# Kernel optimization log

Measured on AMD Instinct MI355X. Metric: run time of the kernel, lower is better.

## Reference

```python
import jax, jax.numpy as jnp
import numpy as np

H = 2048   # hidden_size
I = 4096   # intermediate_size (expert_dim_per_shard, world_size=1)
E = 8      # num_local_experts


def setup_inputs() -> dict:
    key = jax.random.key(0)
    ks = jax.random.split(key, 7)
    s = 0.02
    return {
        "hidden_states": jax.random.normal(ks[0], (1, 2048, H), dtype=jnp.float32),
        "router_w": jax.random.normal(ks[1], (H, E), dtype=jnp.float32) * s,
        "gate_up_proj": jax.random.normal(ks[2], (E, H, 2 * I), dtype=jnp.float32) * s,
        "down_proj": jax.random.normal(ks[3], (E, I, H), dtype=jnp.float32) * s,
        "shared_gate_w": jax.random.normal(ks[4], (H, I), dtype=jnp.float32) * s,
        "shared_up_w": jax.random.normal(ks[5], (H, I), dtype=jnp.float32) * s,
        "shared_down_w": jax.random.normal(ks[6], (I, H), dtype=jnp.float32) * s,
        "top_k": 1,
    }


def reference(hidden_states, router_w, gate_up_proj, down_proj,
              shared_gate_w, shared_up_w, shared_down_w, top_k):
    b, s, h = hidden_states.shape
    hs = hidden_states.reshape(-1, h)                      # [T, H]
    T = hs.shape[0]

    # router + topk scatter (non-topk -> -inf so sigmoid -> 0)
    logits = hs @ router_w                                 # [T, E]
    top_v, top_i = jax.lax.top_k(logits, top_k)            # [T, k]
    neg_inf = jnp.full_like(logits, -jnp.inf)
    rows = jnp.arange(T)[:, None]
    router_scores = neg_inf.at[rows, top_i].set(top_v).T   # [E, T]
    router_scores = jax.nn.sigmoid(router_scores.astype(jnp.float32)).astype(hs.dtype)

    # dense dispatch: every token to every expert, scaled by (mostly zero) scores
    routed_in = hs[None, :, :] * router_scores[:, :, None]  # [E, T, H]

    # per-expert grouped GEMM (SwiGLU)
    gate_up = jnp.einsum('eth,ehf->etf', routed_in, gate_up_proj)  # [E, T, 2I]
    gate, up = jnp.split(gate_up, 2, axis=-1)
    routed_out = jnp.einsum('eti,eih->eth', up * jax.nn.silu(gate), down_proj)  # [E, T, H]

    # shared expert (SwiGLU MLP)
    shared = (jax.nn.silu(hs @ shared_gate_w) * (hs @ shared_up_w)) @ shared_down_w  # [T, H]

    # scatter_add over arange indices == sum over experts
    out = shared + routed_out.sum(axis=0)                  # [T, H]
    return out, router_scores
```

## Files before the change

### kernel.cpp

```cpp
#include <hip/hip_runtime.h>
#include <hip/hip_bf16.h>

#define H_DIM 2048
#define E_NUM 8
#define I_DIM 4096
#define TWO_I 8192
#define T_TOK 2048

#define BM 256
#define BN 64
#define BK 64

typedef __bf16 bf16x8 __attribute__((ext_vector_type(8)));
typedef float f32x4 __attribute__((ext_vector_type(4)));

static __device__ __forceinline__ unsigned short f2bs(float x) {
    __hip_bfloat16 h = __float2bfloat16(x);
    return __builtin_bit_cast(unsigned short, h);
}

#define GLL(gsrc, ldst) __builtin_amdgcn_global_load_lds( \
    (const __attribute__((address_space(1))) void*)(gsrc), \
    (__attribute__((address_space(3))) void*)(ldst), 16, 0, 0)

#define BSWZ(n) (((((n) & 7) ^ (((n) >> 2) & 7))) << 4)

#define A_SRC_CHUNK(lane) ((((lane) & 7) ^ (((lane) >> 3) & 7)) * 8)

static __device__ __forceinline__ void stage_b(
    const float* __restrict__ src, size_t ldb, unsigned short* __restrict__ Bs,
    int wave, int lane) {
    int k0 = wave * 16 + ((lane >> 4) << 2);
    int nb = (lane & 15) << 2;
    const float* p = src + (size_t)k0 * ldb + nb;
    float4 r0 = *reinterpret_cast<const float4*>(p);
    float4 r1 = *reinterpret_cast<const float4*>(p + ldb);
    float4 r2 = *reinterpret_cast<const float4*>(p + 2 * (size_t)ldb);
    float4 r3 = *reinterpret_cast<const float4*>(p + 3 * (size_t)ldb);
    ushort4 o;
    int n, off;
    n = nb + 0;
    o.x = f2bs(r0.x); o.y = f2bs(r1.x); o.z = f2bs(r2.x); o.w = f2bs(r3.x);
    off = (n * 128 + k0 * 2) ^ BSWZ(n);
    *reinterpret_cast<ushort4*>((char*)Bs + off) = o;
    n = nb + 1;
    o.x = f2bs(r0.y); o.y = f2bs(r1.y); o.z = f2bs(r2.y); o.w = f2bs(r3.y);
    off = (n * 128 + k0 * 2) ^ BSWZ(n);
    *reinterpret_cast<ushort4*>((char*)Bs + off) = o;
    n = nb + 2;
    o.x = f2bs(r0.z); o.y = f2bs(r1.z); o.z = f2bs(r2.z); o.w = f2bs(r3.z);
    off = (n * 128 + k0 * 2) ^ BSWZ(n);
    *reinterpret_cast<ushort4*>((char*)Bs + off) = o;
    n = nb + 3;
    o.x = f2bs(r0.w); o.y = f2bs(r1.w); o.z = f2bs(r2.w); o.w = f2bs(r3.w);
    off = (n * 128 + k0 * 2) ^ BSWZ(n);
    *reinterpret_cast<ushort4*>((char*)Bs + off) = o;
}

static __device__ __forceinline__ bf16x8 bload(
    const unsigned short* __restrict__ Bs, int n, int s, int h) {
    int off = (n * 128 + s * 64 + h * 16) ^ BSWZ(n);
    return *reinterpret_cast<const bf16x8*>((const char*)Bs + off);
}

static __device__ __forceinline__ bf16x8 aload(
    const unsigned short* __restrict__ As, int row, int s, int h) {
    int off = row * 128 + ((s * 64 + h * 16) ^ ((row & 7) << 4));
    return *reinterpret_cast<const bf16x8*>((const char*)As + off);
}

__global__ __launch_bounds__(256) void router_convert_kernel(
    const float* __restrict__ hs, const float* __restrict__ rw,
    float* __restrict__ out_scores, int* __restrict__ eidx,
    unsigned short* __restrict__ xb, unsigned short* __restrict__ xs) {
    int tok = blockIdx.x * 4 + (threadIdx.x >> 6);
    int lane = threadIdx.x & 63;
    const float* row = hs + (size_t)tok * H_DIM;
    float4 v[8];
    float acc[E_NUM];
#pragma unroll
    for (int e = 0; e < E_NUM; e++) acc[e] = 0.f;
#pragma unroll
    for (int i = 0; i < 8; i++) {
        int hb = i * 256 + lane * 4;
        v[i] = *reinterpret_cast<const float4*>(row + hb);
        const float* w0 = rw + (size_t)hb * E_NUM;
#pragma unroll
        for (int e = 0; e < E_NUM; e++) {
            acc[e] += v[i].x * w0[e] + v[i].y * w0[E_NUM + e] +
                      v[i].z * w0[2 * E_NUM + e] + v[i].w * w0[3 * E_NUM + e];
        }
    }
#pragma unroll
    for (int e = 0; e < E_NUM; e++) {
#pragma unroll
        for (int o = 32; o > 0; o >>= 1) acc[e] += __shfl_xor(acc[e], o, 64);
    }
    int best = 0; float bv = acc[0];
#pragma unroll
    for (int e = 1; e < E_NUM; e++) { if (acc[e] > bv) { bv = acc[e]; best = e; } }
    float sc = 1.f / (1.f + expf(-bv));
    if (lane < E_NUM) out_scores[(size_t)lane * T_TOK + tok] = (lane == best) ? sc : 0.f;
    if (lane == 0) eidx[tok] = best;
    unsigned short* xbr = xb + (size_t)tok * H_DIM;
    unsigned short* xsr = xs + (size_t)tok * H_DIM;
#pragma unroll
    for (int i = 0; i < 8; i++) {
        int hb = i * 256 + lane * 4;
        ushort4 b, s4;
        b.x = f2bs(v[i].x); b.y = f2bs(v[i].y); b.z = f2bs(v[i].z); b.w = f2bs(v[i].w);
        s4.x = f2bs(v[i].x * sc); s4.y = f2bs(v[i].y * sc);
        s4.z = f2bs(v[i].z * sc); s4.w = f2bs(v[i].w * sc);
        *reinterpret_cast<ushort4*>(xbr + hb) = b;
        *reinterpret_cast<ushort4*>(xsr + hb) = s4;
    }
}

__global__ void group_kernel(const int* __restrict__ eidx, int* __restrict__ perm,
                             int* __restrict__ off) {
    __shared__ int cnt[E_NUM];
    __shared__ int base[E_NUM];
    int t = threadIdx.x;
    if (t < E_NUM) cnt[t] = 0;
    __syncthreads();
    for (int i = t; i < T_TOK; i += 256) atomicAdd(&cnt[eidx[i]], 1);
    __syncthreads();
    if (t == 0) {
        int s = 0;
        for (int e = 0; e < E_NUM; e++) { base[e] = s; off[e] = s; s += cnt[e]; }
        off[E_NUM] = s;
    }
    __syncthreads();
    for (int i = t; i < T_TOK; i += 256) {
        int e = eidx[i];
        int p = atomicAdd(&base[e], 1);
        perm[p] = i;
    }
}

__global__ __launch_bounds__(256, 2) void gemm1_kernel(
    const unsigned short* __restrict__ xb, const unsigned short* __restrict__ xs,
    const float* __restrict__ gup, const float* __restrict__ sg,
    const float* __restrict__ su, const int* __restrict__ perm,
    const int* __restrict__ off, unsigned short* __restrict__ hmid) {
    int nt = blockIdx.x;
    int g = blockIdx.y >> 3;
    int mt = blockIdx.y & 7;
    int rowbase, ng;
    if (g < E_NUM) { rowbase = off[g]; ng = off[g + 1] - rowbase; }
    else { rowbase = 0; ng = T_TOK; }
    int mstart = mt * BM;
    if (mstart >= ng) return;

    __shared__ unsigned short As[BM][BK];
    __shared__ unsigned short Bg[BN * BK];
    __shared__ unsigned short Bu[BN * BK];

    int tid = threadIdx.x;
    int wave = tid >> 6, lane = tid & 63;
    int h = lane >> 4, ln = lane & 15;

    const unsigned short* Abase = (g == E_NUM) ? xb : xs;
    unsigned int aoff[8];
#pragma unroll
    for (int j = 0; j < 8; j++) {
        int r = wave * 64 + j * 8 + (lane >> 3);
        int sr = mstart + r; sr = (sr < ng) ? sr : (ng - 1);
        int tokr = (g < E_NUM) ? perm[rowbase + sr] : sr;
        aoff[j] = (unsigned int)tokr * H_DIM + A_SRC_CHUNK(lane);
    }
    int n0 = nt * BN;
    const float* gbase;
    const float* ubase;
    size_t ldb;
    if (g < E_NUM) {
        gbase = gup + (size_t)g * H_DIM * TWO_I + n0;
        ubase = gbase + I_DIM;
        ldb = TWO_I;
    } else {
        gbase = sg + n0;
        ubase = su + n0;
        ldb = I_DIM;
    }

    f32x4 zero = {0.f, 0.f, 0.f, 0.f};
    f32x4 accg[4][4], accu[4][4];
#pragma unroll
    for (int i = 0; i < 4; i++)
#pragma unroll
        for (int j = 0; j < 4; j++) { accg[i][j] = zero; accu[i][j] = zero; }

    for (int k0 = 0; k0 < H_DIM; k0 += BK) {
#pragma unroll
        for (int j = 0; j < 8; j++) GLL(Abase + aoff[j] + k0, &As[wave * 64 + j * 8][0]);
        stage_b(gbase + (size_t)k0 * ldb, ldb, Bg, wave, lane);
        stage_b(ubase + (size_t)k0 * ldb, ldb, Bu, wave, lane);
        __syncthreads();
#pragma unroll
        for (int s = 0; s < 2; s++) {
            bf16x8 a[4];
#pragma unroll
            for (int i = 0; i < 4; i++)
                a[i] = aload(&As[0][0], wave * 64 + i * 16 + ln, s, h);
#pragma unroll
            for (int j = 0; j < 4; j++) {
                bf16x8 bg = bload(Bg, j * 16 + ln, s, h);
#pragma unroll
                for (int i = 0; i < 4; i++)
                    accg[i][j] = __builtin_amdgcn_mfma_f32_16x16x32_bf16(a[i], bg, accg[i][j], 0, 0, 0);
            }
#pragma unroll
            for (int j = 0; j < 4; j++) {
                bf16x8 bu = bload(Bu, j * 16 + ln, s, h);
#pragma unroll
                for (int i = 0; i < 4; i++)
                    accu[i][j] = __builtin_amdgcn_mfma_f32_16x16x32_bf16(a[i], bu, accu[i][j], 0, 0, 0);
            }
        }
        __syncthreads();
    }
    int hbase = (g < E_NUM) ? rowbase : T_TOK;
#pragma unroll
    for (int i = 0; i < 4; i++) {
#pragma unroll
        for (int j = 0; j < 4; j++) {
#pragma unroll
            for (int r = 0; r < 4; r++) {
                int row = wave * 64 + i * 16 + h * 4 + r;
                int sr = mstart + row;
                if (sr < ng) {
                    float gv = accg[i][j][r], uv = accu[i][j][r];
                    float hv = gv / (1.f + expf(-gv)) * uv;
                    int col = n0 + j * 16 + ln;
                    hmid[(size_t)(hbase + sr) * I_DIM + col] = f2bs(hv);
                }
            }
        }
    }
}

template <int ADD>
__global__ __launch_bounds__(256, 2) void gemm2_kernel(
    const unsigned short* __restrict__ hmid, const float* __restrict__ dwn,
    const float* __restrict__ sd, const int* __restrict__ perm,
    const int* __restrict__ off, float* __restrict__ out) {
    int nt = blockIdx.x;
    int g, mt, rowbase, ng, hbase;
    if (ADD) {
        g = blockIdx.y >> 3; mt = blockIdx.y & 7;
        rowbase = off[g]; ng = off[g + 1] - rowbase; hbase = rowbase;
    } else {
        g = E_NUM; mt = blockIdx.y; rowbase = 0; ng = T_TOK; hbase = T_TOK;
    }
    int mstart = mt * BM;
    if (mstart >= ng) return;

    __shared__ unsigned short As[BM][BK];
    __shared__ unsigned short Bs[BN * BK];

    int tid = threadIdx.x;
    int wave = tid >> 6, lane = tid & 63;
    int h = lane >> 4, ln = lane & 15;

    unsigned int aoff[8];
#pragma unroll
    for (int j = 0; j < 8; j++) {
        int r = wave * 64 + j * 8 + (lane >> 3);
        int sr = mstart + r; sr = (sr < ng) ? sr : (ng - 1);
        aoff[j] = (unsigned int)(hbase + sr) * I_DIM + A_SRC_CHUNK(lane);
    }
    int n0 = nt * BN;
    const float* bbase = ADD ? (dwn + (size_t)g * I_DIM * H_DIM + n0) : (sd + n0);

    f32x4 zero = {0.f, 0.f, 0.f, 0.f};
    f32x4 acc[4][4];
#pragma unroll
    for (int i = 0; i < 4; i++)
#pragma unroll
        for (int j = 0; j < 4; j++) acc[i][j] = zero;

    for (int k0 = 0; k0 < I_DIM; k0 += BK) {
#pragma unroll
        for (int j = 0; j < 8; j++) GLL(hmid + aoff[j] + k0, &As[wave * 64 + j * 8][0]);
        stage_b(bbase + (size_t)k0 * H_DIM, H_DIM, Bs, wave, lane);
        __syncthreads();
#pragma unroll
        for (int s = 0; s < 2; s++) {
            bf16x8 a[4];
#pragma unroll
            for (int i = 0; i < 4; i++)
                a[i] = aload(&As[0][0], wave * 64 + i * 16 + ln, s, h);
#pragma unroll
            for (int j = 0; j < 4; j++) {
                bf16x8 b = bload(Bs, j * 16 + ln, s, h);
#pragma unroll
                for (int i = 0; i < 4; i++)
                    acc[i][j] = __builtin_amdgcn_mfma_f32_16x16x32_bf16(a[i], b, acc[i][j], 0, 0, 0);
            }
        }
        __syncthreads();
    }
#pragma unroll
    for (int i = 0; i < 4; i++) {
#pragma unroll
        for (int j = 0; j < 4; j++) {
#pragma unroll
            for (int r = 0; r < 4; r++) {
                int row = wave * 64 + i * 16 + h * 4 + r;
                int sr = mstart + row;
                if (sr < ng) {
                    int tok = ADD ? perm[rowbase + sr] : sr;
                    int col = n0 + j * 16 + ln;
                    float v = acc[i][j][r];
                    float* o = out + (size_t)tok * H_DIM + col;
                    if (ADD) *o += v; else *o = v;
                }
            }
        }
    }
}

extern "C" void kernel_launch(void* const* d_in, const int* in_sizes, int n_in,
                              void* d_out, int out_size, void* d_ws, size_t ws_size,
                              hipStream_t stream) {
    (void)in_sizes; (void)n_in; (void)out_size;
    const float* hs  = (const float*)d_in[0];
    const float* rw  = (const float*)d_in[1];
    const float* gup = (const float*)d_in[2];
    const float* dwn = (const float*)d_in[3];
    const float* sg  = (const float*)d_in[4];
    const float* su  = (const float*)d_in[5];
    const float* sd  = (const float*)d_in[6];
    float* out = (float*)d_out;
    float* out_scores = out + (size_t)T_TOK * H_DIM;

    char* w = (char*)d_ws;
    size_t o = 0;
    auto alloc = [&](size_t bytes) {
        void* p = w + o;
        o += (bytes + 255) & ~(size_t)255;
        return p;
    };
    unsigned short* xb   = (unsigned short*)alloc((size_t)T_TOK * H_DIM * 2);
    unsigned short* xs   = (unsigned short*)alloc((size_t)T_TOK * H_DIM * 2);
    unsigned short* hmid = (unsigned short*)alloc((size_t)2 * T_TOK * I_DIM * 2);
    int* eidx    = (int*)alloc(T_TOK * 4);
    int* perm    = (int*)alloc(T_TOK * 4);
    int* off     = (int*)alloc(64 * 4);
    if (ws_size < o) return;

    router_convert_kernel<<<T_TOK / 4, 256, 0, stream>>>(hs, rw, out_scores, eidx, xb, xs);
    group_kernel<<<1, 256, 0, stream>>>(eidx, perm, off);

    gemm1_kernel<<<dim3(I_DIM / BN, 9 * 8), 256, 0, stream>>>(
        xb, xs, gup, sg, su, perm, off, hmid);
    gemm2_kernel<0><<<dim3(H_DIM / BN, 8), 256, 0, stream>>>(hmid, dwn, sd, perm, off, out);
    gemm2_kernel<1><<<dim3(H_DIM / BN, E_NUM * 8), 256, 0, stream>>>(hmid, dwn, sd, perm, off, out);
}
```

Baseline: 583.5 us.

## Double-buffer GEMM shared tiles with register prefetch and 512-thread blocks

```diff
diff --git a/kernel.cpp b/kernel.cpp
--- a/kernel.cpp
+++ b/kernel.cpp
@@ -7,10 +7,6 @@
 #define TWO_I 8192
 #define T_TOK 2048
 
-#define BM 256
-#define BN 64
-#define BK 64
-
 typedef __bf16 bf16x8 __attribute__((ext_vector_type(8)));
 typedef float f32x4 __attribute__((ext_vector_type(4)));
 
@@ -24,38 +20,7 @@
     (__attribute__((address_space(3))) void*)(ldst), 16, 0, 0)
 
 #define BSWZ(n) (((((n) & 7) ^ (((n) >> 2) & 7))) << 4)
-
 #define A_SRC_CHUNK(lane) ((((lane) & 7) ^ (((lane) >> 3) & 7)) * 8)
-
-static __device__ __forceinline__ void stage_b(
-    const float* __restrict__ src, size_t ldb, unsigned short* __restrict__ Bs,
-    int wave, int lane) {
-    int k0 = wave * 16 + ((lane >> 4) << 2);
-    int nb = (lane & 15) << 2;
-    const float* p = src + (size_t)k0 * ldb + nb;
-    float4 r0 = *reinterpret_cast<const float4*>(p);
-    float4 r1 = *reinterpret_cast<const float4*>(p + ldb);
-    float4 r2 = *reinterpret_cast<const float4*>(p + 2 * (size_t)ldb);
-    float4 r3 = *reinterpret_cast<const float4*>(p + 3 * (size_t)ldb);
-    ushort4 o;
-    int n, off;
-    n = nb + 0;
-    o.x = f2bs(r0.x); o.y = f2bs(r1.x); o.z = f2bs(r2.x); o.w = f2bs(r3.x);
-    off = (n * 128 + k0 * 2) ^ BSWZ(n);
-    *reinterpret_cast<ushort4*>((char*)Bs + off) = o;
-    n = nb + 1;
-    o.x = f2bs(r0.y); o.y = f2bs(r1.y); o.z = f2bs(r2.y); o.w = f2bs(r3.y);
-    off = (n * 128 + k0 * 2) ^ BSWZ(n);
-    *reinterpret_cast<ushort4*>((char*)Bs + off) = o;
-    n = nb + 2;
-    o.x = f2bs(r0.z); o.y = f2bs(r1.z); o.z = f2bs(r2.z); o.w = f2bs(r3.z);
-    off = (n * 128 + k0 * 2) ^ BSWZ(n);
-    *reinterpret_cast<ushort4*>((char*)Bs + off) = o;
-    n = nb + 3;
-    o.x = f2bs(r0.w); o.y = f2bs(r1.w); o.z = f2bs(r2.w); o.w = f2bs(r3.w);
-    off = (n * 128 + k0 * 2) ^ BSWZ(n);
-    *reinterpret_cast<ushort4*>((char*)Bs + off) = o;
-}
 
 static __device__ __forceinline__ bf16x8 bload(
     const unsigned short* __restrict__ Bs, int n, int s, int h) {
@@ -68,6 +33,8 @@
     int off = row * 128 + ((s * 64 + h * 16) ^ ((row & 7) << 4));
     return *reinterpret_cast<const bf16x8*>((const char*)As + off);
 }
+
+#define MFMA16(a, b, c) __builtin_amdgcn_mfma_f32_16x16x32_bf16(a, b, c, 0, 0, 0)
 
 __global__ __launch_bounds__(256) void router_convert_kernel(
     const float* __restrict__ hs, const float* __restrict__ rw,
@@ -138,7 +105,7 @@
     }
 }
 
-__global__ __launch_bounds__(256, 2) void gemm1_kernel(
+__global__ __launch_bounds__(512, 2) void gemm1_kernel(
     const unsigned short* __restrict__ xb, const unsigned short* __restrict__ xs,
     const float* __restrict__ gup, const float* __restrict__ sg,
     const float* __restrict__ su, const int* __restrict__ perm,
@@ -149,27 +116,28 @@
     int rowbase, ng;
     if (g < E_NUM) { rowbase = off[g]; ng = off[g + 1] - rowbase; }
     else { rowbase = 0; ng = T_TOK; }
-    int mstart = mt * BM;
+    int mstart = mt * 256;
     if (mstart >= ng) return;
 
-    __shared__ unsigned short As[BM][BK];
-    __shared__ unsigned short Bg[BN * BK];
-    __shared__ unsigned short Bu[BN * BK];
+    __shared__ unsigned short As[2][256 * 64];
+    __shared__ unsigned short Bgs[2][64 * 64];
+    __shared__ unsigned short Bus[2][64 * 64];
 
     int tid = threadIdx.x;
     int wave = tid >> 6, lane = tid & 63;
+    int wr = wave >> 1, wc = wave & 1;
     int h = lane >> 4, ln = lane & 15;
 
     const unsigned short* Abase = (g == E_NUM) ? xb : xs;
-    unsigned int aoff[8];
-#pragma unroll
-    for (int j = 0; j < 8; j++) {
-        int r = wave * 64 + j * 8 + (lane >> 3);
+    unsigned int aoff[4];
+#pragma unroll
+    for (int j = 0; j < 4; j++) {
+        int r = wave * 32 + j * 8 + (lane >> 3);
         int sr = mstart + r; sr = (sr < ng) ? sr : (ng - 1);
         int tokr = (g < E_NUM) ? perm[rowbase + sr] : sr;
         aoff[j] = (unsigned int)tokr * H_DIM + A_SRC_CHUNK(lane);
     }
-    int n0 = nt * BN;
+    int n0 = nt * 64;
     const float* gbase;
     const float* ubase;
     size_t ldb;
@@ -182,56 +150,90 @@
         ubase = su + n0;
         ldb = I_DIM;
     }
+    const float* bsrc = (wave < 4) ? gbase : ubase;
+    int bk0 = (wave & 3) * 16 + ((lane >> 4) << 2);
+    int bnb = (lane & 15) << 2;
+    const float* bp = bsrc + (size_t)bk0 * ldb + bnb;
 
     f32x4 zero = {0.f, 0.f, 0.f, 0.f};
-    f32x4 accg[4][4], accu[4][4];
+    f32x4 accg[4][2], accu[4][2];
 #pragma unroll
     for (int i = 0; i < 4; i++)
 #pragma unroll
-        for (int j = 0; j < 4; j++) { accg[i][j] = zero; accu[i][j] = zero; }
-
-    for (int k0 = 0; k0 < H_DIM; k0 += BK) {
-#pragma unroll
-        for (int j = 0; j < 8; j++) GLL(Abase + aoff[j] + k0, &As[wave * 64 + j * 8][0]);
-        stage_b(gbase + (size_t)k0 * ldb, ldb, Bg, wave, lane);
-        stage_b(ubase + (size_t)k0 * ldb, ldb, Bu, wave, lane);
-        __syncthreads();
+        for (int j = 0; j < 2; j++) { accg[i][j] = zero; accu[i][j] = zero; }
+
+    f32x4 q0, q1, q2, q3;
+    const int NT = H_DIM / 64;
+
+#define G1_BLOAD(t) { const float* p_ = bp + (size_t)(t) * 64 * ldb; \
+        q0 = *reinterpret_cast<const f32x4*>(p_); \
+        q1 = *reinterpret_cast<const f32x4*>(p_ + ldb); \
+        q2 = *reinterpret_cast<const f32x4*>(p_ + 2 * ldb); \
+        q3 = *reinterpret_cast<const f32x4*>(p_ + 3 * ldb); }
+#define G1_BWRITE(buf) { char* bdst_ = (char*)((wave < 4) ? &Bgs[buf][0] : &Bus[buf][0]); \
+        _Pragma("unroll") \
+        for (int i_ = 0; i_ < 4; i_++) { int n_ = bnb + i_; ushort4 o_; \
+            o_.x = f2bs(q0[i_]); o_.y = f2bs(q1[i_]); o_.z = f2bs(q2[i_]); o_.w = f2bs(q3[i_]); \
+            int ob_ = (n_ * 128 + bk0 * 2) ^ BSWZ(n_); \
+            *reinterpret_cast<ushort4*>(bdst_ + ob_) = o_; } }
+#define G1_AGLL(t, buf) { _Pragma("unroll") \
+        for (int j_ = 0; j_ < 4; j_++) \
+            GLL(Abase + aoff[j_] + (t) * 64, &As[buf][(wave * 32 + j_ * 8) * 64]); }
+
+    G1_BLOAD(0);
+    G1_AGLL(0, 0);
+    asm volatile("s_waitcnt vmcnt(0)" ::: "memory");
+    G1_BWRITE(0);
+    G1_BLOAD(1);
+    asm volatile("s_waitcnt lgkmcnt(0)" ::: "memory");
+    __builtin_amdgcn_s_barrier();
+
+    int cur = 0;
+    for (int t = 0; t < NT; ++t) {
+        int tn1 = (t + 1 < NT) ? t + 1 : NT - 1;
+        int tn2 = (t + 2 < NT) ? t + 2 : NT - 1;
+        G1_BWRITE(cur ^ 1);
+        G1_AGLL(tn1, cur ^ 1);
+        G1_BLOAD(tn2);
 #pragma unroll
         for (int s = 0; s < 2; s++) {
             bf16x8 a[4];
 #pragma unroll
             for (int i = 0; i < 4; i++)
-                a[i] = aload(&As[0][0], wave * 64 + i * 16 + ln, s, h);
-#pragma unroll
-            for (int j = 0; j < 4; j++) {
-                bf16x8 bg = bload(Bg, j * 16 + ln, s, h);
-#pragma unroll
-                for (int i = 0; i < 4; i++)
-                    accg[i][j] = __builtin_amdgcn_mfma_f32_16x16x32_bf16(a[i], bg, accg[i][j], 0, 0, 0);
+                a[i] = aload(&As[cur][0], wr * 64 + i * 16 + ln, s, h);
+            bf16x8 bg0 = bload(&Bgs[cur][0], wc * 32 + ln, s, h);
+            bf16x8 bg1 = bload(&Bgs[cur][0], wc * 32 + 16 + ln, s, h);
+            bf16x8 bu0 = bload(&Bus[cur][0], wc * 32 + ln, s, h);
+            bf16x8 bu1 = bload(&Bus[cur][0], wc * 32 + 16 + ln, s, h);
+            __builtin_amdgcn_s_setprio(1);
+#pragma unroll
+            for (int i = 0; i < 4; i++) {
+                accg[i][0] = MFMA16(a[i], bg0, accg[i][0]);
+                accg[i][1] = MFMA16(a[i], bg1, accg[i][1]);
+                accu[i][0] = MFMA16(a[i], bu0, accu[i][0]);
+                accu[i][1] = MFMA16(a[i], bu1, accu[i][1]);
             }
-#pragma unroll
-            for (int j = 0; j < 4; j++) {
-                bf16x8 bu = bload(Bu, j * 16 + ln, s, h);
-#pragma unroll
-                for (int i = 0; i < 4; i++)
-                    accu[i][j] = __builtin_amdgcn_mfma_f32_16x16x32_bf16(a[i], bu, accu[i][j], 0, 0, 0);
-            }
+            __builtin_amdgcn_s_setprio(0);
         }
-        __syncthreads();
-    }
+        asm volatile("s_waitcnt vmcnt(4)" ::: "memory");
+        asm volatile("s_waitcnt lgkmcnt(0)" ::: "memory");
+        __builtin_amdgcn_s_barrier();
+        cur ^= 1;
+    }
+
     int hbase = (g < E_NUM) ? rowbase : T_TOK;
 #pragma unroll
     for (int i = 0; i < 4; i++) {
 #pragma unroll
-        for (int j = 0; j < 4; j++) {
+        for (int jj = 0; jj < 2; jj++) {
 #pragma unroll
             for (int r = 0; r < 4; r++) {
-                int row = wave * 64 + i * 16 + h * 4 + r;
+                int row = wr * 64 + i * 16 + h * 4 + r;
                 int sr = mstart + row;
                 if (sr < ng) {
-                    float gv = accg[i][j][r], uv = accu[i][j][r];
+                    float gv = accg[i][jj][r], uv = accu[i][jj][r];
                     float hv = gv / (1.f + expf(-gv)) * uv;
-                    int col = n0 + j * 16 + ln;
+                    int col = n0 + wc * 32 + jj * 16 + ln;
                     hmid[(size_t)(hbase + sr) * I_DIM + col] = f2bs(hv);
                 }
             }
@@ -240,7 +242,7 @@
 }
 
 template <int ADD>
-__global__ __launch_bounds__(256, 2) void gemm2_kernel(
+__global__ __launch_bounds__(512, 2) void gemm2_kernel(
     const unsigned short* __restrict__ hmid, const float* __restrict__ dwn,
     const float* __restrict__ sd, const int* __restrict__ perm,
     const int* __restrict__ off, float* __restrict__ out) {
@@ -252,25 +254,29 @@
     } else {
         g = E_NUM; mt = blockIdx.y; rowbase = 0; ng = T_TOK; hbase = T_TOK;
     }
-    int mstart = mt * BM;
+    int mstart = mt * 256;
     if (mstart >= ng) return;
 
-    __shared__ unsigned short As[BM][BK];
-    __shared__ unsigned short Bs[BN * BK];
+    __shared__ unsigned short As[2][256 * 64];
+    __shared__ unsigned short Bs[2][128 * 64];
 
     int tid = threadIdx.x;
     int wave = tid >> 6, lane = tid & 63;
+    int wr = wave >> 1, wc = wave & 1;
     int h = lane >> 4, ln = lane & 15;
 
-    unsigned int aoff[8];
-#pragma unroll
-    for (int j = 0; j < 8; j++) {
-        int r = wave * 64 + j * 8 + (lane >> 3);
+    unsigned int aoff[4];
+#pragma unroll
+    for (int j = 0; j < 4; j++) {
+        int r = wave * 32 + j * 8 + (lane >> 3);
         int sr = mstart + r; sr = (sr < ng) ? sr : (ng - 1);
         aoff[j] = (unsigned int)(hbase + sr) * I_DIM + A_SRC_CHUNK(lane);
     }
-    int n0 = nt * BN;
+    int n0 = nt * 128;
     const float* bbase = ADD ? (dwn + (size_t)g * I_DIM * H_DIM + n0) : (sd + n0);
+    int bk0 = ((tid >> 5) & 15) * 4;
+    int bnb = (tid & 31) * 4;
+    const float* bp = bbase + (size_t)bk0 * H_DIM + bnb;
 
     f32x4 zero = {0.f, 0.f, 0.f, 0.f};
     f32x4 acc[4][4];
@@ -279,38 +285,74 @@
 #pragma unroll
         for (int j = 0; j < 4; j++) acc[i][j] = zero;
 
-    for (int k0 = 0; k0 < I_DIM; k0 += BK) {
-#pragma unroll
-        for (int j = 0; j < 8; j++) GLL(hmid + aoff[j] + k0, &As[wave * 64 + j * 8][0]);
-        stage_b(bbase + (size_t)k0 * H_DIM, H_DIM, Bs, wave, lane);
-        __syncthreads();
+    f32x4 q0, q1, q2, q3;
+    const int NT = I_DIM / 64;
+
+#define G2_BLOAD(t) { const float* p_ = bp + (size_t)(t) * 64 * H_DIM; \
+        q0 = *reinterpret_cast<const f32x4*>(p_); \
+        q1 = *reinterpret_cast<const f32x4*>(p_ + H_DIM); \
+        q2 = *reinterpret_cast<const f32x4*>(p_ + 2 * H_DIM); \
+        q3 = *reinterpret_cast<const f32x4*>(p_ + 3 * H_DIM); }
+#define G2_BWRITE(buf) { char* bdst_ = (char*)&Bs[buf][0]; \
+        _Pragma("unroll") \
+        for (int i_ = 0; i_ < 4; i_++) { int n_ = bnb + i_; ushort4 o_; \
+            o_.x = f2bs(q0[i_]); o_.y = f2bs(q1[i_]); o_.z = f2bs(q2[i_]); o_.w = f2bs(q3[i_]); \
+            int ob_ = (n_ * 128 + bk0 * 2) ^ BSWZ(n_); \
+            *reinterpret_cast<ushort4*>(bdst_ + ob_) = o_; } }
+#define G2_AGLL(t, buf) { _Pragma("unroll") \
+        for (int j_ = 0; j_ < 4; j_++) \
+            GLL(hmid + aoff[j_] + (t) * 64, &As[buf][(wave * 32 + j_ * 8) * 64]); }
+
+    G2_BLOAD(0);
+    G2_AGLL(0, 0);
+    asm volatile("s_waitcnt vmcnt(0)" ::: "memory");
+    G2_BWRITE(0);
+    G2_BLOAD(1);
+    asm volatile("s_waitcnt lgkmcnt(0)" ::: "memory");
+    __builtin_amdgcn_s_barrier();
+
+    int cur = 0;
+    for (int t = 0; t < NT; ++t) {
+        int tn1 = (t + 1 < NT) ? t + 1 : NT - 1;
+        int tn2 = (t + 2 < NT) ? t + 2 : NT - 1;
+        G2_BWRITE(cur ^ 1);
+        G2_AGLL(tn1, cur ^ 1);
+        G2_BLOAD(tn2);
 #pragma unroll
         for (int s = 0; s < 2; s++) {
             bf16x8 a[4];
 #pragma unroll
             for (int i = 0; i < 4; i++)
-                a[i] = aload(&As[0][0], wave * 64 + i * 16 + ln, s, h);
-#pragma unroll
-            for (int j = 0; j < 4; j++) {
-                bf16x8 b = bload(Bs, j * 16 + ln, s, h);
+                a[i] = aload(&As[cur][0], wr * 64 + i * 16 + ln, s, h);
+            bf16x8 b[4];
+#pragma unroll
+            for (int j = 0; j < 4; j++)
+                b[j] = bload(&Bs[cur][0], wc * 64 + j * 16 + ln, s, h);
+            __builtin_amdgcn_s_setprio(1);
+#pragma unroll
+            for (int j = 0; j < 4; j++)
 #pragma unroll
                 for (int i = 0; i < 4; i++)
-                    acc[i][j] = __builtin_amdgcn_mfma_f32_16x16x32_bf16(a[i], b, acc[i][j], 0, 0, 0);
-            }
+                    acc[i][j] = MFMA16(a[i], b[j], acc[i][j]);
+            __builtin_amdgcn_s_setprio(0);
         }
-        __syncthreads();
-    }
+        asm volatile("s_waitcnt vmcnt(4)" ::: "memory");
+        asm volatile("s_waitcnt lgkmcnt(0)" ::: "memory");
+        __builtin_amdgcn_s_barrier();
+        cur ^= 1;
+    }
+
 #pragma unroll
     for (int i = 0; i < 4; i++) {
 #pragma unroll
         for (int j = 0; j < 4; j++) {
 #pragma unroll
             for (int r = 0; r < 4; r++) {
-                int row = wave * 64 + i * 16 + h * 4 + r;
+                int row = wr * 64 + i * 16 + h * 4 + r;
                 int sr = mstart + row;
                 if (sr < ng) {
                     int tok = ADD ? perm[rowbase + sr] : sr;
-                    int col = n0 + j * 16 + ln;
+                    int col = n0 + wc * 64 + j * 16 + ln;
                     float v = acc[i][j][r];
                     float* o = out + (size_t)tok * H_DIM + col;
                     if (ADD) *o += v; else *o = v;
@@ -352,8 +394,8 @@
     router_convert_kernel<<<T_TOK / 4, 256, 0, stream>>>(hs, rw, out_scores, eidx, xb, xs);
     group_kernel<<<1, 256, 0, stream>>>(eidx, perm, off);
 
-    gemm1_kernel<<<dim3(I_DIM / BN, 9 * 8), 256, 0, stream>>>(
+    gemm1_kernel<<<dim3(I_DIM / 64, 9 * 8), 512, 0, stream>>>(
         xb, xs, gup, sg, su, perm, off, hmid);
-    gemm2_kernel<0><<<dim3(H_DIM / BN, 8), 256, 0, stream>>>(hmid, dwn, sd, perm, off, out);
-    gemm2_kernel<1><<<dim3(H_DIM / BN, E_NUM * 8), 256, 0, stream>>>(hmid, dwn, sd, perm, off, out);
-}
+    gemm2_kernel<0><<<dim3(H_DIM / 128, 8), 512, 0, stream>>>(hmid, dwn, sd, perm, off, out);
+    gemm2_kernel<1><<<dim3(H_DIM / 128, E_NUM * 8), 512, 0, stream>>>(hmid, dwn, sd, perm, off, out);
+}
```

Result: slower. 636.9 us (+9.2%).

## Replace LDS-staged GEMMs with direct-to-register loads and register prefetch

Applied to the files above, without the earlier changes.

```diff
diff --git a/kernel.cpp b/kernel.cpp
--- a/kernel.cpp
+++ b/kernel.cpp
@@ -7,10 +7,6 @@
 #define TWO_I 8192
 #define T_TOK 2048
 
-#define BM 256
-#define BN 64
-#define BK 64
-
 typedef __bf16 bf16x8 __attribute__((ext_vector_type(8)));
 typedef float f32x4 __attribute__((ext_vector_type(4)));
 
@@ -19,55 +15,17 @@
     return __builtin_bit_cast(unsigned short, h);
 }
 
-#define GLL(gsrc, ldst) __builtin_amdgcn_global_load_lds( \
-    (const __attribute__((address_space(1))) void*)(gsrc), \
-    (__attribute__((address_space(3))) void*)(ldst), 16, 0, 0)
-
-#define BSWZ(n) (((((n) & 7) ^ (((n) >> 2) & 7))) << 4)
-
-#define A_SRC_CHUNK(lane) ((((lane) & 7) ^ (((lane) >> 3) & 7)) * 8)
-
-static __device__ __forceinline__ void stage_b(
-    const float* __restrict__ src, size_t ldb, unsigned short* __restrict__ Bs,
-    int wave, int lane) {
-    int k0 = wave * 16 + ((lane >> 4) << 2);
-    int nb = (lane & 15) << 2;
-    const float* p = src + (size_t)k0 * ldb + nb;
-    float4 r0 = *reinterpret_cast<const float4*>(p);
-    float4 r1 = *reinterpret_cast<const float4*>(p + ldb);
-    float4 r2 = *reinterpret_cast<const float4*>(p + 2 * (size_t)ldb);
-    float4 r3 = *reinterpret_cast<const float4*>(p + 3 * (size_t)ldb);
-    ushort4 o;
-    int n, off;
-    n = nb + 0;
-    o.x = f2bs(r0.x); o.y = f2bs(r1.x); o.z = f2bs(r2.x); o.w = f2bs(r3.x);
-    off = (n * 128 + k0 * 2) ^ BSWZ(n);
-    *reinterpret_cast<ushort4*>((char*)Bs + off) = o;
-    n = nb + 1;
-    o.x = f2bs(r0.y); o.y = f2bs(r1.y); o.z = f2bs(r2.y); o.w = f2bs(r3.y);
-    off = (n * 128 + k0 * 2) ^ BSWZ(n);
-    *reinterpret_cast<ushort4*>((char*)Bs + off) = o;
-    n = nb + 2;
-    o.x = f2bs(r0.z); o.y = f2bs(r1.z); o.z = f2bs(r2.z); o.w = f2bs(r3.z);
-    off = (n * 128 + k0 * 2) ^ BSWZ(n);
-    *reinterpret_cast<ushort4*>((char*)Bs + off) = o;
-    n = nb + 3;
-    o.x = f2bs(r0.w); o.y = f2bs(r1.w); o.z = f2bs(r2.w); o.w = f2bs(r3.w);
-    off = (n * 128 + k0 * 2) ^ BSWZ(n);
-    *reinterpret_cast<ushort4*>((char*)Bs + off) = o;
-}
-
-static __device__ __forceinline__ bf16x8 bload(
-    const unsigned short* __restrict__ Bs, int n, int s, int h) {
-    int off = (n * 128 + s * 64 + h * 16) ^ BSWZ(n);
-    return *reinterpret_cast<const bf16x8*>((const char*)Bs + off);
-}
-
-static __device__ __forceinline__ bf16x8 aload(
-    const unsigned short* __restrict__ As, int row, int s, int h) {
-    int off = row * 128 + ((s * 64 + h * 16) ^ ((row & 7) << 4));
-    return *reinterpret_cast<const bf16x8*>((const char*)As + off);
-}
+static __device__ __forceinline__ bf16x8 cvt8(const float* q) {
+    bf16x8 r;
+#pragma unroll
+    for (int j = 0; j < 8; j++) r[j] = (__bf16)q[j];
+    return r;
+}
+
+#define MFMA16(a, b, c) __builtin_amdgcn_mfma_f32_16x16x32_bf16(a, b, c, 0, 0, 0)
+
+#define LDQ(dst, p, kk) { _Pragma("unroll") \
+    for (int j_ = 0; j_ < 8; j_++) dst[j_] = (p)[(kk) + (size_t)j_ * ldb]; }
 
 __global__ __launch_bounds__(256) void router_convert_kernel(
     const float* __restrict__ hs, const float* __restrict__ rw,
@@ -138,101 +96,90 @@
     }
 }
 
-__global__ __launch_bounds__(256, 2) void gemm1_kernel(
+__global__ __launch_bounds__(256, 3) void gemm1_kernel(
     const unsigned short* __restrict__ xb, const unsigned short* __restrict__ xs,
     const float* __restrict__ gup, const float* __restrict__ sg,
     const float* __restrict__ su, const int* __restrict__ perm,
     const int* __restrict__ off, unsigned short* __restrict__ hmid) {
     int nt = blockIdx.x;
-    int g = blockIdx.y >> 3;
-    int mt = blockIdx.y & 7;
+    int g = blockIdx.y >> 4;
+    int mt = blockIdx.y & 15;
     int rowbase, ng;
     if (g < E_NUM) { rowbase = off[g]; ng = off[g + 1] - rowbase; }
     else { rowbase = 0; ng = T_TOK; }
-    int mstart = mt * BM;
+    int mstart = mt * 128;
     if (mstart >= ng) return;
-
-    __shared__ unsigned short As[BM][BK];
-    __shared__ unsigned short Bg[BN * BK];
-    __shared__ unsigned short Bu[BN * BK];
 
     int tid = threadIdx.x;
     int wave = tid >> 6, lane = tid & 63;
-    int h = lane >> 4, ln = lane & 15;
+    int wr = wave >> 1, wc = wave & 1;
+    int ln = lane & 15, h = lane >> 4;
 
     const unsigned short* Abase = (g == E_NUM) ? xb : xs;
-    unsigned int aoff[8];
-#pragma unroll
-    for (int j = 0; j < 8; j++) {
-        int r = wave * 64 + j * 8 + (lane >> 3);
-        int sr = mstart + r; sr = (sr < ng) ? sr : (ng - 1);
-        int tokr = (g < E_NUM) ? perm[rowbase + sr] : sr;
-        aoff[j] = (unsigned int)tokr * H_DIM + A_SRC_CHUNK(lane);
-    }
-    int n0 = nt * BN;
-    const float* gbase;
-    const float* ubase;
-    size_t ldb;
-    if (g < E_NUM) {
-        gbase = gup + (size_t)g * H_DIM * TWO_I + n0;
-        ubase = gbase + I_DIM;
-        ldb = TWO_I;
-    } else {
-        gbase = sg + n0;
-        ubase = su + n0;
-        ldb = I_DIM;
-    }
+    int mbase = mstart + wr * 64;
+    unsigned aoff0, aoff1, aoff2, aoff3;
+#define MKAOFF1(i, dst) { int r_ = mbase + i * 16 + ln; r_ = (r_ < ng) ? r_ : (ng - 1); \
+        int tok_ = (g < E_NUM) ? perm[rowbase + r_] : r_; dst = (unsigned)tok_ * H_DIM + h * 8; }
+    MKAOFF1(0, aoff0) MKAOFF1(1, aoff1) MKAOFF1(2, aoff2) MKAOFF1(3, aoff3)
+
+    const float* gbase; const float* ubase; size_t ldb;
+    if (g < E_NUM) { gbase = gup + (size_t)g * H_DIM * TWO_I; ubase = gbase + I_DIM; ldb = TWO_I; }
+    else { gbase = sg; ubase = su; ldb = I_DIM; }
+    int colg = nt * 64 + wc * 32 + ln;
+    const float* pg0 = gbase + (size_t)(h * 8) * ldb + colg;
+    const float* pg1 = pg0 + 16;
+    const float* pu0 = ubase + (size_t)(h * 8) * ldb + colg;
+    const float* pu1 = pu0 + 16;
 
     f32x4 zero = {0.f, 0.f, 0.f, 0.f};
-    f32x4 accg[4][4], accu[4][4];
+    f32x4 accg[4][2], accu[4][2];
 #pragma unroll
     for (int i = 0; i < 4; i++)
 #pragma unroll
-        for (int j = 0; j < 4; j++) { accg[i][j] = zero; accu[i][j] = zero; }
-
-    for (int k0 = 0; k0 < H_DIM; k0 += BK) {
-#pragma unroll
-        for (int j = 0; j < 8; j++) GLL(Abase + aoff[j] + k0, &As[wave * 64 + j * 8][0]);
-        stage_b(gbase + (size_t)k0 * ldb, ldb, Bg, wave, lane);
-        stage_b(ubase + (size_t)k0 * ldb, ldb, Bu, wave, lane);
-        __syncthreads();
-#pragma unroll
-        for (int s = 0; s < 2; s++) {
-            bf16x8 a[4];
-#pragma unroll
-            for (int i = 0; i < 4; i++)
-                a[i] = aload(&As[0][0], wave * 64 + i * 16 + ln, s, h);
-#pragma unroll
-            for (int j = 0; j < 4; j++) {
-                bf16x8 bg = bload(Bg, j * 16 + ln, s, h);
-#pragma unroll
-                for (int i = 0; i < 4; i++)
-                    accg[i][j] = __builtin_amdgcn_mfma_f32_16x16x32_bf16(a[i], bg, accg[i][j], 0, 0, 0);
-            }
-#pragma unroll
-            for (int j = 0; j < 4; j++) {
-                bf16x8 bu = bload(Bu, j * 16 + ln, s, h);
-#pragma unroll
-                for (int i = 0; i < 4; i++)
-                    accu[i][j] = __builtin_amdgcn_mfma_f32_16x16x32_bf16(a[i], bu, accu[i][j], 0, 0, 0);
-            }
-        }
-        __syncthreads();
-    }
+        for (int j = 0; j < 2; j++) { accg[i][j] = zero; accu[i][j] = zero; }
+
+    float qg0[8], qg1[8], qu0[8], qu1[8];
+    bf16x8 aq0, aq1, aq2, aq3;
+    const int NT = H_DIM / 32;
+
+    LDQ(qg0, pg0, 0); LDQ(qg1, pg1, 0); LDQ(qu0, pu0, 0); LDQ(qu1, pu1, 0);
+    aq0 = *(const bf16x8*)(Abase + aoff0);
+    aq1 = *(const bf16x8*)(Abase + aoff1);
+    aq2 = *(const bf16x8*)(Abase + aoff2);
+    aq3 = *(const bf16x8*)(Abase + aoff3);
+
+    for (int t = 0; t < NT; ++t) {
+        bf16x8 bg0 = cvt8(qg0), bg1 = cvt8(qg1), bu0 = cvt8(qu0), bu1 = cvt8(qu1);
+        bf16x8 a0 = aq0, a1 = aq1, a2 = aq2, a3 = aq3;
+        int tn = (t + 1 < NT) ? (t + 1) : t;
+        size_t kk = (size_t)tn * 32 * ldb;
+        unsigned ka = (unsigned)tn * 32;
+        LDQ(qg0, pg0, kk); LDQ(qg1, pg1, kk); LDQ(qu0, pu0, kk); LDQ(qu1, pu1, kk);
+        aq0 = *(const bf16x8*)(Abase + aoff0 + ka);
+        aq1 = *(const bf16x8*)(Abase + aoff1 + ka);
+        aq2 = *(const bf16x8*)(Abase + aoff2 + ka);
+        aq3 = *(const bf16x8*)(Abase + aoff3 + ka);
+#define G1_ROW(i, ai) \
+        accg[i][0] = MFMA16(ai, bg0, accg[i][0]); \
+        accg[i][1] = MFMA16(ai, bg1, accg[i][1]); \
+        accu[i][0] = MFMA16(ai, bu0, accu[i][0]); \
+        accu[i][1] = MFMA16(ai, bu1, accu[i][1]);
+        G1_ROW(0, a0) G1_ROW(1, a1) G1_ROW(2, a2) G1_ROW(3, a3)
+    }
+
     int hbase = (g < E_NUM) ? rowbase : T_TOK;
 #pragma unroll
     for (int i = 0; i < 4; i++) {
 #pragma unroll
-        for (int j = 0; j < 4; j++) {
+        for (int jn = 0; jn < 2; jn++) {
 #pragma unroll
             for (int r = 0; r < 4; r++) {
-                int row = wave * 64 + i * 16 + h * 4 + r;
-                int sr = mstart + row;
-                if (sr < ng) {
-                    float gv = accg[i][j][r], uv = accu[i][j][r];
+                int row = mbase + i * 16 + h * 4 + r;
+                if (row < ng) {
+                    float gv = accg[i][jn][r], uv = accu[i][jn][r];
                     float hv = gv / (1.f + expf(-gv)) * uv;
-                    int col = n0 + j * 16 + ln;
-                    hmid[(size_t)(hbase + sr) * I_DIM + col] = f2bs(hv);
+                    int col = nt * 64 + wc * 32 + jn * 16 + ln;
+                    hmid[(size_t)(hbase + row) * I_DIM + col] = f2bs(hv);
                 }
             }
         }
@@ -240,37 +187,39 @@
 }
 
 template <int ADD>
-__global__ __launch_bounds__(256, 2) void gemm2_kernel(
+__global__ __launch_bounds__(256, 3) void gemm2_kernel(
     const unsigned short* __restrict__ hmid, const float* __restrict__ dwn,
     const float* __restrict__ sd, const int* __restrict__ perm,
     const int* __restrict__ off, float* __restrict__ out) {
     int nt = blockIdx.x;
     int g, mt, rowbase, ng, hbase;
     if (ADD) {
-        g = blockIdx.y >> 3; mt = blockIdx.y & 7;
+        g = blockIdx.y >> 4; mt = blockIdx.y & 15;
         rowbase = off[g]; ng = off[g + 1] - rowbase; hbase = rowbase;
     } else {
         g = E_NUM; mt = blockIdx.y; rowbase = 0; ng = T_TOK; hbase = T_TOK;
     }
-    int mstart = mt * BM;
+    int mstart = mt * 128;
     if (mstart >= ng) return;
-
-    __shared__ unsigned short As[BM][BK];
-    __shared__ unsigned short Bs[BN * BK];
 
     int tid = threadIdx.x;
     int wave = tid >> 6, lane = tid & 63;
-    int h = lane >> 4, ln = lane & 15;
-
-    unsigned int aoff[8];
-#pragma unroll
-    for (int j = 0; j < 8; j++) {
-        int r = wave * 64 + j * 8 + (lane >> 3);
-        int sr = mstart + r; sr = (sr < ng) ? sr : (ng - 1);
-        aoff[j] = (unsigned int)(hbase + sr) * I_DIM + A_SRC_CHUNK(lane);
-    }
-    int n0 = nt * BN;
-    const float* bbase = ADD ? (dwn + (size_t)g * I_DIM * H_DIM + n0) : (sd + n0);
+    int wr = wave >> 1, wc = wave & 1;
+    int ln = lane & 15, h = lane >> 4;
+
+    int mbase = mstart + wr * 64;
+    unsigned aoff0, aoff1, aoff2, aoff3;
+#define MKAOFF2(i, dst) { int r_ = mbase + i * 16 + ln; r_ = (r_ < ng) ? r_ : (ng - 1); \
+        dst = (unsigned)(hbase + r_) * I_DIM + h * 8; }
+    MKAOFF2(0, aoff0) MKAOFF2(1, aoff1) MKAOFF2(2, aoff2) MKAOFF2(3, aoff3)
+
+    const float* bbase = ADD ? (dwn + (size_t)g * I_DIM * H_DIM) : sd;
+    const size_t ldb = H_DIM;
+    int coln = nt * 128 + wc * 64 + ln;
+    const float* pb0 = bbase + (size_t)(h * 8) * ldb + coln;
+    const float* pb1 = pb0 + 16;
+    const float* pb2 = pb0 + 32;
+    const float* pb3 = pb0 + 48;
 
     f32x4 zero = {0.f, 0.f, 0.f, 0.f};
     f32x4 acc[4][4];
@@ -279,38 +228,45 @@
 #pragma unroll
         for (int j = 0; j < 4; j++) acc[i][j] = zero;
 
-    for (int k0 = 0; k0 < I_DIM; k0 += BK) {
-#pragma unroll
-        for (int j = 0; j < 8; j++) GLL(hmid + aoff[j] + k0, &As[wave * 64 + j * 8][0]);
-        stage_b(bbase + (size_t)k0 * H_DIM, H_DIM, Bs, wave, lane);
-        __syncthreads();
-#pragma unroll
-        for (int s = 0; s < 2; s++) {
-            bf16x8 a[4];
-#pragma unroll
-            for (int i = 0; i < 4; i++)
-                a[i] = aload(&As[0][0], wave * 64 + i * 16 + ln, s, h);
-#pragma unroll
-            for (int j = 0; j < 4; j++) {
-                bf16x8 b = bload(Bs, j * 16 + ln, s, h);
-#pragma unroll
-                for (int i = 0; i < 4; i++)
-                    acc[i][j] = __builtin_amdgcn_mfma_f32_16x16x32_bf16(a[i], b, acc[i][j], 0, 0, 0);
-            }
-        }
-        __syncthreads();
-    }
+    float qb0[8], qb1[8], qb2[8], qb3[8];
+    bf16x8 aq0, aq1, aq2, aq3;
+    const int NT = I_DIM / 32;
+
+    LDQ(qb0, pb0, 0); LDQ(qb1, pb1, 0); LDQ(qb2, pb2, 0); LDQ(qb3, pb3, 0);
+    aq0 = *(const bf16x8*)(hmid + aoff0);
+    aq1 = *(const bf16x8*)(hmid + aoff1);
+    aq2 = *(const bf16x8*)(hmid + aoff2);
+    aq3 = *(const bf16x8*)(hmid + aoff3);
+
+    for (int t = 0; t < NT; ++t) {
+        bf16x8 b0 = cvt8(qb0), b1 = cvt8(qb1), b2 = cvt8(qb2), b3 = cvt8(qb3);
+        bf16x8 a0 = aq0, a1 = aq1, a2 = aq2, a3 = aq3;
+        int tn = (t + 1 < NT) ? (t + 1) : t;
+        size_t kk = (size_t)tn * 32 * ldb;
+        unsigned ka = (unsigned)tn * 32;
+        LDQ(qb0, pb0, kk); LDQ(qb1, pb1, kk); LDQ(qb2, pb2, kk); LDQ(qb3, pb3, kk);
+        aq0 = *(const bf16x8*)(hmid + aoff0 + ka);
+        aq1 = *(const bf16x8*)(hmid + aoff1 + ka);
+        aq2 = *(const bf16x8*)(hmid + aoff2 + ka);
+        aq3 = *(const bf16x8*)(hmid + aoff3 + ka);
+#define G2_ROW(i, ai) \
+        acc[i][0] = MFMA16(ai, b0, acc[i][0]); \
+        acc[i][1] = MFMA16(ai, b1, acc[i][1]); \
+        acc[i][2] = MFMA16(ai, b2, acc[i][2]); \
+        acc[i][3] = MFMA16(ai, b3, acc[i][3]);
+        G2_ROW(0, a0) G2_ROW(1, a1) G2_ROW(2, a2) G2_ROW(3, a3)
+    }
+
 #pragma unroll
     for (int i = 0; i < 4; i++) {
 #pragma unroll
         for (int j = 0; j < 4; j++) {
 #pragma unroll
             for (int r = 0; r < 4; r++) {
-                int row = wave * 64 + i * 16 + h * 4 + r;
-                int sr = mstart + row;
-                if (sr < ng) {
-                    int tok = ADD ? perm[rowbase + sr] : sr;
-                    int col = n0 + j * 16 + ln;
+                int row = mbase + i * 16 + h * 4 + r;
+                if (row < ng) {
+                    int tok = ADD ? perm[rowbase + row] : row;
+                    int col = nt * 128 + wc * 64 + j * 16 + ln;
                     float v = acc[i][j][r];
                     float* o = out + (size_t)tok * H_DIM + col;
                     if (ADD) *o += v; else *o = v;
@@ -352,8 +308,8 @@
     router_convert_kernel<<<T_TOK / 4, 256, 0, stream>>>(hs, rw, out_scores, eidx, xb, xs);
     group_kernel<<<1, 256, 0, stream>>>(eidx, perm, off);
 
-    gemm1_kernel<<<dim3(I_DIM / BN, 9 * 8), 256, 0, stream>>>(
+    gemm1_kernel<<<dim3(I_DIM / 64, 9 * 16), 256, 0, stream>>>(
         xb, xs, gup, sg, su, perm, off, hmid);
-    gemm2_kernel<0><<<dim3(H_DIM / BN, 8), 256, 0, stream>>>(hmid, dwn, sd, perm, off, out);
-    gemm2_kernel<1><<<dim3(H_DIM / BN, E_NUM * 8), 256, 0, stream>>>(hmid, dwn, sd, perm, off, out);
-}
+    gemm2_kernel<0><<<dim3(H_DIM / 128, 16), 256, 0, stream>>>(hmid, dwn, sd, perm, off, out);
+    gemm2_kernel<1><<<dim3(H_DIM / 128, E_NUM * 16), 256, 0, stream>>>(hmid, dwn, sd, perm, off, out);
+}
```

After: 1.062 ms. 81.9% more time.

## Software-pipeline both GEMM kernels with double-buffered A and register-prefetched B

Applied to the files above, without the earlier changes.

```diff
diff --git a/kernel.cpp b/kernel.cpp
--- a/kernel.cpp
+++ b/kernel.cpp
@@ -23,39 +23,10 @@
     (const __attribute__((address_space(1))) void*)(gsrc), \
     (__attribute__((address_space(3))) void*)(ldst), 16, 0, 0)
 
+#define MFMA16(a, b, c) __builtin_amdgcn_mfma_f32_16x16x32_bf16(a, b, c, 0, 0, 0)
 #define BSWZ(n) (((((n) & 7) ^ (((n) >> 2) & 7))) << 4)
-
 #define A_SRC_CHUNK(lane) ((((lane) & 7) ^ (((lane) >> 3) & 7)) * 8)
-
-static __device__ __forceinline__ void stage_b(
-    const float* __restrict__ src, size_t ldb, unsigned short* __restrict__ Bs,
-    int wave, int lane) {
-    int k0 = wave * 16 + ((lane >> 4) << 2);
-    int nb = (lane & 15) << 2;
-    const float* p = src + (size_t)k0 * ldb + nb;
-    float4 r0 = *reinterpret_cast<const float4*>(p);
-    float4 r1 = *reinterpret_cast<const float4*>(p + ldb);
-    float4 r2 = *reinterpret_cast<const float4*>(p + 2 * (size_t)ldb);
-    float4 r3 = *reinterpret_cast<const float4*>(p + 3 * (size_t)ldb);
-    ushort4 o;
-    int n, off;
-    n = nb + 0;
-    o.x = f2bs(r0.x); o.y = f2bs(r1.x); o.z = f2bs(r2.x); o.w = f2bs(r3.x);
-    off = (n * 128 + k0 * 2) ^ BSWZ(n);
-    *reinterpret_cast<ushort4*>((char*)Bs + off) = o;
-    n = nb + 1;
-    o.x = f2bs(r0.y); o.y = f2bs(r1.y); o.z = f2bs(r2.y); o.w = f2bs(r3.y);
-    off = (n * 128 + k0 * 2) ^ BSWZ(n);
-    *reinterpret_cast<ushort4*>((char*)Bs + off) = o;
-    n = nb + 2;
-    o.x = f2bs(r0.z); o.y = f2bs(r1.z); o.z = f2bs(r2.z); o.w = f2bs(r3.z);
-    off = (n * 128 + k0 * 2) ^ BSWZ(n);
-    *reinterpret_cast<ushort4*>((char*)Bs + off) = o;
-    n = nb + 3;
-    o.x = f2bs(r0.w); o.y = f2bs(r1.w); o.z = f2bs(r2.w); o.w = f2bs(r3.w);
-    off = (n * 128 + k0 * 2) ^ BSWZ(n);
-    *reinterpret_cast<ushort4*>((char*)Bs + off) = o;
-}
+#define BARRIER() asm volatile("s_waitcnt lgkmcnt(0)\ns_barrier" ::: "memory")
 
 static __device__ __forceinline__ bf16x8 bload(
     const unsigned short* __restrict__ Bs, int n, int s, int h) {
@@ -152,7 +123,7 @@
     int mstart = mt * BM;
     if (mstart >= ng) return;
 
-    __shared__ unsigned short As[BM][BK];
+    __shared__ unsigned short As[2][BM * BK];
     __shared__ unsigned short Bg[BN * BK];
     __shared__ unsigned short Bu[BN * BK];
 
@@ -182,6 +153,10 @@
         ubase = su + n0;
         ldb = I_DIM;
     }
+    int k0i = wave * 16 + ((lane >> 4) << 2);
+    int nb = (lane & 15) << 2;
+    const float* pg = gbase + (size_t)k0i * ldb + nb;
+    const float* pu = ubase + (size_t)k0i * ldb + nb;
 
     f32x4 zero = {0.f, 0.f, 0.f, 0.f};
     f32x4 accg[4][4], accu[4][4];
@@ -190,35 +165,78 @@
 #pragma unroll
         for (int j = 0; j < 4; j++) { accg[i][j] = zero; accu[i][j] = zero; }
 
-    for (int k0 = 0; k0 < H_DIM; k0 += BK) {
-#pragma unroll
-        for (int j = 0; j < 8; j++) GLL(Abase + aoff[j] + k0, &As[wave * 64 + j * 8][0]);
-        stage_b(gbase + (size_t)k0 * ldb, ldb, Bg, wave, lane);
-        stage_b(ubase + (size_t)k0 * ldb, ldb, Bu, wave, lane);
-        __syncthreads();
+    const int NT = H_DIM / BK;
+    f32x4 qg0, qg1, qg2, qg3, qu0, qu1, qu2, qu3;
+
+#define G1_QLOAD(t_) { size_t ko_ = (size_t)(t_) * BK * ldb; \
+        const float* p_ = pg + ko_; \
+        qg0 = *reinterpret_cast<const f32x4*>(p_); \
+        qg1 = *reinterpret_cast<const f32x4*>(p_ + ldb); \
+        qg2 = *reinterpret_cast<const f32x4*>(p_ + 2 * ldb); \
+        qg3 = *reinterpret_cast<const f32x4*>(p_ + 3 * ldb); \
+        p_ = pu + ko_; \
+        qu0 = *reinterpret_cast<const f32x4*>(p_); \
+        qu1 = *reinterpret_cast<const f32x4*>(p_ + ldb); \
+        qu2 = *reinterpret_cast<const f32x4*>(p_ + 2 * ldb); \
+        qu3 = *reinterpret_cast<const f32x4*>(p_ + 3 * ldb); }
+#define G1_BWRITE() { _Pragma("unroll") \
+        for (int i_ = 0; i_ < 4; i_++) { int n_ = nb + i_; \
+            ushort4 og_, ou_; \
+            og_.x = f2bs(qg0[i_]); og_.y = f2bs(qg1[i_]); \
+            og_.z = f2bs(qg2[i_]); og_.w = f2bs(qg3[i_]); \
+            ou_.x = f2bs(qu0[i_]); ou_.y = f2bs(qu1[i_]); \
+            ou_.z = f2bs(qu2[i_]); ou_.w = f2bs(qu3[i_]); \
+            int ob_ = (n_ * 128 + k0i * 2) ^ BSWZ(n_); \
+            *reinterpret_cast<ushort4*>((char*)Bg + ob_) = og_; \
+            *reinterpret_cast<ushort4*>((char*)Bu + ob_) = ou_; } }
+#define G1_AGLL(t_, buf_) { _Pragma("unroll") \
+        for (int j_ = 0; j_ < 8; j_++) \
+            GLL(Abase + aoff[j_] + (unsigned)(t_) * BK, \
+                &As[buf_][(wave * 64 + j_ * 8) * BK]); }
+
+    G1_QLOAD(0);
+    G1_AGLL(0, 0);
+    asm volatile("s_waitcnt vmcnt(0)" ::: "memory");
+    G1_BWRITE();
+    G1_AGLL(1, 1);
+    G1_QLOAD(1);
+    BARRIER();
+
+    for (int t = 0; t < NT; ++t) {
+        const unsigned short* Ab = &As[t & 1][0];
 #pragma unroll
         for (int s = 0; s < 2; s++) {
-            bf16x8 a[4];
-#pragma unroll
-            for (int i = 0; i < 4; i++)
-                a[i] = aload(&As[0][0], wave * 64 + i * 16 + ln, s, h);
+            bf16x8 a0 = aload(Ab, wave * 64 + 0 * 16 + ln, s, h);
+            bf16x8 a1 = aload(Ab, wave * 64 + 1 * 16 + ln, s, h);
+            bf16x8 a2 = aload(Ab, wave * 64 + 2 * 16 + ln, s, h);
+            bf16x8 a3 = aload(Ab, wave * 64 + 3 * 16 + ln, s, h);
 #pragma unroll
             for (int j = 0; j < 4; j++) {
                 bf16x8 bg = bload(Bg, j * 16 + ln, s, h);
-#pragma unroll
-                for (int i = 0; i < 4; i++)
-                    accg[i][j] = __builtin_amdgcn_mfma_f32_16x16x32_bf16(a[i], bg, accg[i][j], 0, 0, 0);
+                accg[0][j] = MFMA16(a0, bg, accg[0][j]);
+                accg[1][j] = MFMA16(a1, bg, accg[1][j]);
+                accg[2][j] = MFMA16(a2, bg, accg[2][j]);
+                accg[3][j] = MFMA16(a3, bg, accg[3][j]);
             }
 #pragma unroll
             for (int j = 0; j < 4; j++) {
                 bf16x8 bu = bload(Bu, j * 16 + ln, s, h);
-#pragma unroll
-                for (int i = 0; i < 4; i++)
-                    accu[i][j] = __builtin_amdgcn_mfma_f32_16x16x32_bf16(a[i], bu, accu[i][j], 0, 0, 0);
+                accu[0][j] = MFMA16(a0, bu, accu[0][j]);
+                accu[1][j] = MFMA16(a1, bu, accu[1][j]);
+                accu[2][j] = MFMA16(a2, bu, accu[2][j]);
+                accu[3][j] = MFMA16(a3, bu, accu[3][j]);
             }
         }
-        __syncthreads();
-    }
+        BARRIER();
+        if (t + 1 < NT) {
+            G1_BWRITE();
+            int tc = t + 2; if (tc > NT - 1) tc = NT - 1;
+            G1_AGLL(tc, t & 1);
+            G1_QLOAD(tc);
+            BARRIER();
+        }
+    }
+
     int hbase = (g < E_NUM) ? rowbase : T_TOK;
 #pragma unroll
     for (int i = 0; i < 4; i++) {
@@ -255,7 +273,7 @@
     int mstart = mt * BM;
     if (mstart >= ng) return;
 
-    __shared__ unsigned short As[BM][BK];
+    __shared__ unsigned short As[2][BM * BK];
     __shared__ unsigned short Bs[BN * BK];
 
     int tid = threadIdx.x;
@@ -271,6 +289,10 @@
     }
     int n0 = nt * BN;
     const float* bbase = ADD ? (dwn + (size_t)g * I_DIM * H_DIM + n0) : (sd + n0);
+    const size_t ldb = H_DIM;
+    int k0i = wave * 16 + ((lane >> 4) << 2);
+    int nb = (lane & 15) << 2;
+    const float* pb = bbase + (size_t)k0i * ldb + nb;
 
     f32x4 zero = {0.f, 0.f, 0.f, 0.f};
     f32x4 acc[4][4];
@@ -279,27 +301,62 @@
 #pragma unroll
         for (int j = 0; j < 4; j++) acc[i][j] = zero;
 
-    for (int k0 = 0; k0 < I_DIM; k0 += BK) {
-#pragma unroll
-        for (int j = 0; j < 8; j++) GLL(hmid + aoff[j] + k0, &As[wave * 64 + j * 8][0]);
-        stage_b(bbase + (size_t)k0 * H_DIM, H_DIM, Bs, wave, lane);
-        __syncthreads();
+    const int NT2 = I_DIM / BK;
+    f32x4 qb0, qb1, qb2, qb3;
+
+#define G2_QLOAD(t_) { size_t ko_ = (size_t)(t_) * BK * ldb; \
+        const float* p_ = pb + ko_; \
+        qb0 = *reinterpret_cast<const f32x4*>(p_); \
+        qb1 = *reinterpret_cast<const f32x4*>(p_ + ldb); \
+        qb2 = *reinterpret_cast<const f32x4*>(p_ + 2 * ldb); \
+        qb3 = *reinterpret_cast<const f32x4*>(p_ + 3 * ldb); }
+#define G2_BWRITE() { _Pragma("unroll") \
+        for (int i_ = 0; i_ < 4; i_++) { int n_ = nb + i_; \
+            ushort4 o_; \
+            o_.x = f2bs(qb0[i_]); o_.y = f2bs(qb1[i_]); \
+            o_.z = f2bs(qb2[i_]); o_.w = f2bs(qb3[i_]); \
+            int ob_ = (n_ * 128 + k0i * 2) ^ BSWZ(n_); \
+            *reinterpret_cast<ushort4*>((char*)Bs + ob_) = o_; } }
+#define G2_AGLL(t_, buf_) { _Pragma("unroll") \
+        for (int j_ = 0; j_ < 8; j_++) \
+            GLL(hmid + aoff[j_] + (unsigned)(t_) * BK, \
+                &As[buf_][(wave * 64 + j_ * 8) * BK]); }
+
+    G2_QLOAD(0);
+    G2_AGLL(0, 0);
+    asm volatile("s_waitcnt vmcnt(0)" ::: "memory");
+    G2_BWRITE();
+    G2_AGLL(1, 1);
+    G2_QLOAD(1);
+    BARRIER();
+
+    for (int t = 0; t < NT2; ++t) {
+        const unsigned short* Ab = &As[t & 1][0];
 #pragma unroll
         for (int s = 0; s < 2; s++) {
-            bf16x8 a[4];
-#pragma unroll
-            for (int i = 0; i < 4; i++)
-                a[i] = aload(&As[0][0], wave * 64 + i * 16 + ln, s, h);
+            bf16x8 a0 = aload(Ab, wave * 64 + 0 * 16 + ln, s, h);
+            bf16x8 a1 = aload(Ab, wave * 64 + 1 * 16 + ln, s, h);
+            bf16x8 a2 = aload(Ab, wave * 64 + 2 * 16 + ln, s, h);
+            bf16x8 a3 = aload(Ab, wave * 64 + 3 * 16 + ln, s, h);
 #pragma unroll
             for (int j = 0; j < 4; j++) {
                 bf16x8 b = bload(Bs, j * 16 + ln, s, h);
-#pragma unroll
-                for (int i = 0; i < 4; i++)
-                    acc[i][j] = __builtin_amdgcn_mfma_f32_16x16x32_bf16(a[i], b, acc[i][j], 0, 0, 0);
+                acc[0][j] = MFMA16(a0, b, acc[0][j]);
+                acc[1][j] = MFMA16(a1, b, acc[1][j]);
+                acc[2][j] = MFMA16(a2, b, acc[2][j]);
+                acc[3][j] = MFMA16(a3, b, acc[3][j]);
             }
         }
-        __syncthreads();
-    }
+        BARRIER();
+        if (t + 1 < NT2) {
+            G2_BWRITE();
+            int tc = t + 2; if (tc > NT2 - 1) tc = NT2 - 1;
+            G2_AGLL(tc, t & 1);
+            G2_QLOAD(tc);
+            BARRIER();
+        }
+    }
+
 #pragma unroll
     for (int i = 0; i < 4; i++) {
 #pragma unroll
```

After: 507.9 us. 12.9% less time.
